# Kernel tuning notes

Measured on AMD Instinct MI355X. Metric: run time of the kernel, lower is better.

## Reference

```python
import jax, jax.numpy as jnp
import numpy as np

B, S, D_IN, UNITS = 8, 2048, 512, 512


def _glorot(key, fan_in, fan_out):
    limit = np.sqrt(6.0 / (fan_in + fan_out)).astype(np.float32)
    return jax.random.uniform(key, (fan_in, fan_out), jnp.float32, -limit, limit)


def setup_inputs() -> dict:
    key = jax.random.key(0)
    kq, kwq, kwv, kwk = jax.random.split(key, 4)
    return {
        "query": jax.random.normal(kq, (B, S, D_IN), jnp.float32),
        "Wq": _glorot(kwq, D_IN, UNITS),   # W_query conv1d k=1, no bias
        "Wv": _glorot(kwv, D_IN, UNITS),   # W_value conv1d k=1, no bias
        "Wk": _glorot(kwk, D_IN, UNITS),   # W_key   conv1d k=1, no bias
    }


def reference(query, Wq, Wv, Wk):
    # Pointwise causal Conv1D(kernel=1, no bias) with sigmoid activation == sigmoid(x @ W)
    q = jax.nn.sigmoid(jnp.einsum('bsd,du->bsu', query, Wq))   # W_query(query)
    k = jax.nn.sigmoid(jnp.einsum('bsd,du->bsu', query, Wv))   # W_value(key=query)
    v = jax.nn.sigmoid(jnp.einsum('bsd,du->bsu', query, Wk))   # W_key(value=query)

    d_in = query.shape[-1]  # scaling uses value's input feature dim, not units
    score = jnp.einsum('bqu,bku->bqk', q, k) / jnp.sqrt(jnp.float32(d_in))  # [B,S,S]

    # Mask: upper triangle INCLUDING diagonal is -inf (strictly-causal, no self)
    s = score.shape[1]
    masked = jnp.where(jnp.triu(jnp.ones((s, s), bool)), -jnp.inf, score)

    # Row 0 is fully masked -> replaced by zeros; rows 1: softmax over j < i
    rest = jax.nn.softmax(masked[:, 1:, :], axis=-1)
    attn = jnp.concatenate([jnp.zeros((score.shape[0], 1, s), score.dtype), rest], axis=1)

    return jnp.einsum('bqk,bku->bqu', attn, v)
```

## Files before the change

kernel.cpp:

```cpp
#include <hip/hip_runtime.h>
#include <stdint.h>


typedef __attribute__((ext_vector_type(4))) float f32x4;
typedef __attribute__((ext_vector_type(8))) short short8;
typedef __attribute__((ext_vector_type(4))) short short4b;

__device__ __forceinline__ short f2bf(float f) {
    union { float f; uint32_t u; } v; v.f = f;
    uint32_t r = (v.u + 0x7FFFu + ((v.u >> 16) & 1u)) >> 16;
    return (short)r;
}
__device__ __forceinline__ float bf2f(short s) {
    union { uint32_t u; float f; } v; v.u = ((uint32_t)(uint16_t)s) << 16; return v.f;
}
__device__ __forceinline__ float sigm(float x) { return 1.0f / (1.0f + __expf(-x)); }

__device__ __forceinline__ void gload_lds16(const void* g, void* l) {
    __builtin_amdgcn_global_load_lds(
        (const __attribute__((address_space(1))) void*)g,
        (__attribute__((address_space(3))) void*)l, 16, 0, 0);
}

#define VMBAR() asm volatile("s_waitcnt vmcnt(0)\n\ts_barrier" ::: "memory")

__global__ __launch_bounds__(256) void convert_x(
    const float* __restrict__ X, short* __restrict__ Xb)
{
    size_t i = (size_t)blockIdx.x * 256 + threadIdx.x;
    const float4* src = reinterpret_cast<const float4*>(X) + i * 2;
    float4 a = src[0], b = src[1];
    short8 o;
    o[0] = f2bf(a.x); o[1] = f2bf(a.y); o[2] = f2bf(a.z); o[3] = f2bf(a.w);
    o[4] = f2bf(b.x); o[5] = f2bf(b.y); o[6] = f2bf(b.z); o[7] = f2bf(b.w);
    *reinterpret_cast<short8*>(Xb + i * 8) = o;
}

__global__ __launch_bounds__(256) void prep_weights(
    const float* __restrict__ Wq, const float* __restrict__ Wv, const float* __restrict__ Wk,
    short* __restrict__ Wt)
{
    __shared__ float T[64 * 68];
    int bid = blockIdx.x;
    int w = bid >> 6;
    int tile = bid & 63;
    int n0 = (tile & 7) * 64;
    int k0 = (tile >> 3) * 64;
    const float* W = (w == 0) ? Wq : (w == 1) ? Wv : Wk;
    int t = threadIdx.x;
    int tr = t >> 4, tc = t & 15;
    for (int rr = 0; rr < 4; ++rr) {
        int row = rr * 16 + tr;
        float4 v = *reinterpret_cast<const float4*>(&W[(size_t)(k0 + row) * 512 + n0 + tc * 4]);
        T[row * 68 + tc * 4 + 0] = v.x;
        T[row * 68 + tc * 4 + 1] = v.y;
        T[row * 68 + tc * 4 + 2] = v.z;
        T[row * 68 + tc * 4 + 3] = v.w;
    }
    __syncthreads();
    for (int wr = 0; wr < 4; ++wr) {
        int nl = wr * 16 + tr;
        short4b o;
        for (int i = 0; i < 4; ++i) o[i] = f2bf(T[(tc * 4 + i) * 68 + nl]);
        *reinterpret_cast<short4b*>(&Wt[((size_t)(w * 512 + n0 + nl)) * 512 + k0 + tc * 4]) = o;
    }
}

__global__ __launch_bounds__(512, 1) void qkv_gemm(
    const short* __restrict__ Xb,
    const short* __restrict__ Wt,
    short* __restrict__ Qb, short* __restrict__ Kb, short* __restrict__ VtG)
{
    __shared__ short SMEM[2][24576];

    int bid = blockIdx.x;
    int xcd = bid & 7;
    int r5 = bid >> 3;
    int mt = xcd * 16 + (r5 & 15);
    int y2 = r5 >> 4;
    int m0 = mt * 128;
    int n2 = y2 * 256;

    int tid = threadIdx.x;
    int wv = tid >> 6, lane = tid & 63;
    int wm = wv >> 2, wn = wv & 3;
    int ln = lane & 15, hi = lane >> 4;

    f32x4 acc[4][4];
#pragma unroll
    for (int i = 0; i < 4; ++i)
#pragma unroll
        for (int j = 0; j < 4; ++j) acc[i][j] = {0.f, 0.f, 0.f, 0.f};

    const short* Asrc = Xb + (size_t)m0 * 512;
    const short* Bsrc = Wt + (size_t)n2 * 512;

#define STAGE(ko, buf)                                                             \
    {                                                                              \
        int _k0 = (ko) * 64;                                                       \
        _Pragma("unroll")                                                          \
        for (int _j = 0; _j < 2; ++_j) {                                           \
            int _r0 = wv * 16 + _j * 8;                                            \
            int _r = _r0 + (lane >> 3);                                            \
            int _sc = ((lane & 7) * 8) ^ ((_r & 7) << 3);                          \
            gload_lds16(Asrc + (size_t)_r * 512 + _k0 + _sc,                       \
                        &SMEM[buf][_r0 * 64]);                                     \
        }                                                                          \
        _Pragma("unroll")                                                          \
        for (int _j = 0; _j < 4; ++_j) {                                           \
            int _r0 = wv * 32 + _j * 8;                                            \
            int _r = _r0 + (lane >> 3);                                            \
            int _sc = ((lane & 7) * 8) ^ ((_r & 7) << 3);                          \
            gload_lds16(Bsrc + (size_t)_r * 512 + _k0 + _sc,                       \
                        &SMEM[buf][8192 + _r0 * 64]);                              \
        }                                                                          \
    }

    STAGE(0, 0);
    for (int ko = 0; ko < 8; ++ko) {
        VMBAR();
        if (ko + 1 < 8) STAGE(ko + 1, (ko + 1) & 1);
        const short* As = SMEM[ko & 1];
        const short* Bs = SMEM[ko & 1] + 8192;
#pragma unroll
        for (int kk = 0; kk < 2; ++kk) {
            int kof = kk * 32 + hi * 8;
            int sw = (ln & 7) << 3;
            short8 af[4], bf[4];
#pragma unroll
            for (int mf = 0; mf < 4; ++mf) {
                int rr = wm * 64 + mf * 16 + ln;
                af[mf] = *reinterpret_cast<const short8*>(&As[rr * 64 + (kof ^ sw)]);
            }
#pragma unroll
            for (int nf = 0; nf < 4; ++nf) {
                int rr = wn * 64 + nf * 16 + ln;
                bf[nf] = *reinterpret_cast<const short8*>(&Bs[rr * 64 + (kof ^ sw)]);
            }
#pragma unroll
            for (int mf = 0; mf < 4; ++mf)
#pragma unroll
                for (int nf = 0; nf < 4; ++nf)
                    acc[mf][nf] = __builtin_amdgcn_mfma_f32_16x16x32_bf16(af[mf], bf[nf], acc[mf][nf], 0, 0, 0);
        }
    }
    __syncthreads();
#undef STAGE

    int w2 = n2 >> 9;
    int nc = n2 & 511;
    short* Ts = SMEM[0];

    if (w2 < 2) {
#pragma unroll
        for (int mf = 0; mf < 4; ++mf)
#pragma unroll
            for (int nf = 0; nf < 4; ++nf)
#pragma unroll
                for (int j = 0; j < 4; ++j) {
                    int rl = wm * 64 + mf * 16 + hi * 4 + j;
                    int cl = wn * 64 + nf * 16 + ln;
                    Ts[rl * 256 + (cl ^ ((rl & 7) << 3))] = f2bf(sigm(acc[mf][nf][j]));
                }
        __syncthreads();
        short* O = (w2 == 0) ? Qb : Kb;
        int rr = tid >> 2, h = tid & 3;
#pragma unroll
        for (int i = 0; i < 8; ++i) {
            int c8 = h * 64 + i * 8;
            short8 v = *reinterpret_cast<const short8*>(&Ts[rr * 256 + (c8 ^ ((rr & 7) << 3))]);
            *reinterpret_cast<short8*>(&O[(size_t)(m0 + rr) * 512 + nc + c8]) = v;
        }
    } else {
#pragma unroll
        for (int mf = 0; mf < 4; ++mf)
#pragma unroll
            for (int nf = 0; nf < 4; ++nf)
#pragma unroll
                for (int j = 0; j < 4; ++j) {
                    int sl = wm * 64 + mf * 16 + hi * 4 + j;
                    int dl = wn * 64 + nf * 16 + ln;
                    Ts[dl * 128 + (sl ^ ((dl & 7) << 3))] = f2bf(sigm(acc[mf][nf][j]));
                }
        __syncthreads();
        int bb = m0 >> 11;
        int s0 = m0 & 2047;
        int d = tid >> 1, h = tid & 1;
#pragma unroll
        for (int i = 0; i < 8; ++i) {
            int s8 = h * 64 + i * 8;
            short8 v = *reinterpret_cast<const short8*>(&Ts[d * 128 + (s8 ^ ((d & 7) << 3))]);
            *reinterpret_cast<short8*>(&VtG[((size_t)(bb * 512 + nc + d)) * 2048 + s0 + s8]) = v;
        }
    }
}

__global__ __launch_bounds__(256, 2) void score_pass(
    const short* __restrict__ Qb, const short* __restrict__ Kb,
    short* __restrict__ Pc, float* __restrict__ Dpart)
{
    __shared__ short SMEM[2][16384];
    __shared__ float psum[2][128];

    const float scale = 0.044194173824159216f;

    int bid = blockIdx.x;
    int b = bid & 7;
    int idx = bid >> 3;
    int ti = 0;
    while ((ti + 1) * (ti + 2) / 2 <= idx) ++ti;
    int tj = idx - ti * (ti + 1) / 2;
    int m0 = ti * 128, n0 = tj * 128;

    int tid = threadIdx.x;
    int w = tid >> 6, lane = tid & 63;
    int wr = w >> 1, wc = w & 1;
    int ln = lane & 15, hi = lane >> 4;

    const short* Qsrc = Qb + (size_t)b * 2048 * 512 + (size_t)m0 * 512;
    const short* Ksrc = Kb + (size_t)b * 2048 * 512 + (size_t)n0 * 512;

    f32x4 acc[4][4];
#pragma unroll
    for (int i = 0; i < 4; ++i)
#pragma unroll
        for (int j = 0; j < 4; ++j) acc[i][j] = {0.f, 0.f, 0.f, 0.f};

    int srow = w * 8 + (lane >> 3);
    int ssc0 = (lane & 7) * 8;

#define SSTAGE(ko, buf)                                                            \
    {                                                                              \
        int _k0 = (ko) * 64;                                                       \
        _Pragma("unroll")                                                          \
        for (int _j = 0; _j < 4; ++_j) {                                           \
            int _r = srow + _j * 32;                                               \
            int _sc = ssc0 ^ ((_r & 7) << 3);                                      \
            gload_lds16(Qsrc + (size_t)_r * 512 + _k0 + _sc,                       \
                        &SMEM[buf][(w * 8 + _j * 32) * 64]);                       \
        }                                                                          \
        _Pragma("unroll")                                                          \
        for (int _j = 0; _j < 4; ++_j) {                                           \
            int _r = srow + _j * 32;                                               \
            int _sc = ssc0 ^ ((_r & 7) << 3);                                      \
            gload_lds16(Ksrc + (size_t)_r * 512 + _k0 + _sc,                       \
                        &SMEM[buf][8192 + (w * 8 + _j * 32) * 64]);                \
        }                                                                          \
    }

    SSTAGE(0, 0);
    for (int ko = 0; ko < 8; ++ko) {
        VMBAR();
        if (ko + 1 < 8) SSTAGE(ko + 1, (ko + 1) & 1);
        const short* As = SMEM[ko & 1];
        const short* Bs = SMEM[ko & 1] + 8192;
#pragma unroll
        for (int kk = 0; kk < 2; ++kk) {
            int kof = kk * 32 + hi * 8;
            int sw = (ln & 7) << 3;
            short8 af[4], bf[4];
#pragma unroll
            for (int mf = 0; mf < 4; ++mf)
                af[mf] = *reinterpret_cast<const short8*>(&As[(wr * 64 + mf * 16 + ln) * 64 + (kof ^ sw)]);
#pragma unroll
            for (int nf = 0; nf < 4; ++nf)
                bf[nf] = *reinterpret_cast<const short8*>(&Bs[(wc * 64 + nf * 16 + ln) * 64 + (kof ^ sw)]);
#pragma unroll
            for (int mf = 0; mf < 4; ++mf)
#pragma unroll
                for (int nf = 0; nf < 4; ++nf)
                    acc[mf][nf] = __builtin_amdgcn_mfma_f32_16x16x32_bf16(af[mf], bf[nf], acc[mf][nf], 0, 0, 0);
        }
    }
    __syncthreads();
#undef SSTAGE

    short* Ts = SMEM[0];
#pragma unroll
    for (int mf = 0; mf < 4; ++mf) {
        float rs[4] = {0.f, 0.f, 0.f, 0.f};
#pragma unroll
        for (int nf = 0; nf < 4; ++nf)
#pragma unroll
            for (int j = 0; j < 4; ++j) {
                int rl = wr * 64 + mf * 16 + hi * 4 + j;
                int cl = wc * 64 + nf * 16 + ln;
                int irow = m0 + rl, jcol = n0 + cl;
                float p = (jcol < irow) ? __expf(acc[mf][nf][j] * scale) : 0.f;
                short hs = f2bf(p);
                Ts[rl * 128 + (cl ^ ((rl & 7) << 3))] = hs;
                rs[j] += bf2f(hs);
            }
#pragma unroll
        for (int j = 0; j < 4; ++j) {
            float s = rs[j];
            s += __shfl_xor(s, 1);
            s += __shfl_xor(s, 2);
            s += __shfl_xor(s, 4);
            s += __shfl_xor(s, 8);
            if (ln == 0) psum[wc][wr * 64 + mf * 16 + hi * 4 + j] = s;
        }
    }
    __syncthreads();
    short* Ptile = Pc + (size_t)(b * 136 + idx) * 128 * 128;
    {
        int r = tid >> 1, h = tid & 1;
#pragma unroll
        for (int i = 0; i < 8; ++i) {
            int c8 = h * 64 + i * 8;
            short8 v = *reinterpret_cast<const short8*>(&Ts[r * 128 + (c8 ^ ((r & 7) << 3))]);
            *reinterpret_cast<short8*>(&Ptile[(size_t)r * 128 + c8]) = v;
        }
    }
    if (tid < 128)
        Dpart[((size_t)b * 16 + tj) * 2048 + m0 + tid] = psum[0][tid] + psum[1][tid];
}

__global__ __launch_bounds__(256) void pv_pass(
    const short* __restrict__ Pc, const short* __restrict__ VtG,
    const float* __restrict__ Dpart, float* __restrict__ Out)
{
    __shared__ short SMEM[2][12288];
    __shared__ float dnm[128];

    int bid = blockIdx.x;
    int b = bid & 7;
    int rr = bid >> 3;
    int grp = rr >> 5, off = rr & 31;
    int ti = (grp & 1) ? (15 - (off >> 1)) : (off >> 1);
    int colhalf = 2 * grp + (off & 1);
    int m0 = ti * 128, n0 = colhalf * 64;

    int tid = threadIdx.x;
    int w = tid >> 6, lane = tid & 63;
    int wr = w >> 1, wc = w & 1;
    int ln = lane & 15, hi = lane >> 4;

    if (tid < 128) {
        float s = 0.f;
        for (int tj = 0; tj <= ti; ++tj)
            s += Dpart[((size_t)b * 16 + tj) * 2048 + m0 + tid];
        int gi = m0 + tid;
        dnm[tid] = (gi == 0) ? 0.f : 1.0f / s;
    }

    const short* Ptiles = Pc + (size_t)(b * 136 + ti * (ti + 1) / 2) * 128 * 128;
    const short* Vsrc = VtG + (size_t)b * 512 * 2048 + (size_t)n0 * 2048;

    f32x4 acc[4][2];
#pragma unroll
    for (int i = 0; i < 4; ++i)
#pragma unroll
        for (int j = 0; j < 2; ++j) acc[i][j] = {0.f, 0.f, 0.f, 0.f};

    int srow = w * 8 + (lane >> 3);
    int ssc0 = (lane & 7) * 8;
    int nks = 2 * (ti + 1);

#define PSTAGE(ks, buf)                                                            \
    {                                                                              \
        int _tj = (ks) >> 1;                                                       \
        int _j0 = ((ks) & 1) * 64;                                                 \
        const short* _Pt = Ptiles + (size_t)_tj * 128 * 128;                       \
        _Pragma("unroll")                                                          \
        for (int _j = 0; _j < 4; ++_j) {                                           \
            int _r = srow + _j * 32;                                               \
            int _sc = ssc0 ^ ((_r & 7) << 3);                                      \
            gload_lds16(_Pt + (size_t)_r * 128 + _j0 + _sc,                        \
                        &SMEM[buf][(w * 8 + _j * 32) * 64]);                       \
        }                                                                          \
        _Pragma("unroll")                                                          \
        for (int _j = 0; _j < 2; ++_j) {                                           \
            int _r = srow + _j * 32;                                               \
            int _sc = ssc0 ^ ((_r & 7) << 3);                                      \
            gload_lds16(Vsrc + (size_t)_r * 2048 + _tj * 128 + _j0 + _sc,          \
                        &SMEM[buf][8192 + (w * 8 + _j * 32) * 64]);                \
        }                                                                          \
    }

    PSTAGE(0, 0);
    for (int ks = 0; ks < nks; ++ks) {
        VMBAR();
        if (ks + 1 < nks) PSTAGE(ks + 1, (ks + 1) & 1);
        const short* As = SMEM[ks & 1];
        const short* Bs = SMEM[ks & 1] + 8192;
#pragma unroll
        for (int kk = 0; kk < 2; ++kk) {
            int kof = kk * 32 + hi * 8;
            int sw = (ln & 7) << 3;
            short8 af[4], bf[2];
#pragma unroll
            for (int mf = 0; mf < 4; ++mf)
                af[mf] = *reinterpret_cast<const short8*>(&As[(wr * 64 + mf * 16 + ln) * 64 + (kof ^ sw)]);
#pragma unroll
            for (int nf = 0; nf < 2; ++nf)
                bf[nf] = *reinterpret_cast<const short8*>(&Bs[(wc * 32 + nf * 16 + ln) * 64 + (kof ^ sw)]);
#pragma unroll
            for (int mf = 0; mf < 4; ++mf)
#pragma unroll
                for (int nf = 0; nf < 2; ++nf)
                    acc[mf][nf] = __builtin_amdgcn_mfma_f32_16x16x32_bf16(af[mf], bf[nf], acc[mf][nf], 0, 0, 0);
        }
    }
    __syncthreads();
#undef PSTAGE

    float* Tf = reinterpret_cast<float*>(SMEM);
#pragma unroll
    for (int mf = 0; mf < 4; ++mf)
#pragma unroll
        for (int nf = 0; nf < 2; ++nf)
#pragma unroll
            for (int j = 0; j < 4; ++j) {
                int rl = wr * 64 + mf * 16 + hi * 4 + j;
                int cl = wc * 32 + nf * 16 + ln;
                Tf[rl * 64 + (cl ^ ((rl & 7) << 2))] = acc[mf][nf][j] * dnm[rl];
            }
    __syncthreads();
    {
        int r = tid >> 1, h = tid & 1;
        float* orow = Out + ((size_t)b * 2048 + m0 + r) * 512 + n0;
#pragma unroll
        for (int i = 0; i < 8; ++i) {
            int c4 = (h * 8 + i) * 4;
            float4 v = *reinterpret_cast<const float4*>(&Tf[r * 64 + (c4 ^ ((r & 7) << 2))]);
            *reinterpret_cast<float4*>(&orow[c4]) = v;
        }
    }
}

extern "C" void kernel_launch(void* const* d_in, const int* in_sizes, int n_in,
                              void* d_out, int out_size, void* d_ws, size_t ws_size,
                              hipStream_t stream) {
    const float* X  = (const float*)d_in[0];
    const float* Wq = (const float*)d_in[1];
    const float* Wv = (const float*)d_in[2];
    const float* Wk = (const float*)d_in[3];
    float* Out = (float*)d_out;

    char* ws = (char*)d_ws;
    const size_t WT_BYTES  = (size_t)3 * 512 * 512 * 2;
    const size_t MAT_BYTES = (size_t)16384 * 512 * 2;
    const size_t PC_BYTES  = (size_t)8 * 136 * 128 * 128 * 2;
    short* Wt = (short*)ws;
    short* Qb = (short*)(ws + WT_BYTES);
    short* Kb = (short*)(ws + WT_BYTES + MAT_BYTES);
    short* Vt = (short*)(ws + WT_BYTES + 2 * MAT_BYTES);
    short* Pc = (short*)(ws + WT_BYTES + 3 * MAT_BYTES);
    short* Xb = Pc;
    float* Dp = (float*)(ws + WT_BYTES + 3 * MAT_BYTES + PC_BYTES);

    convert_x<<<4096, 256, 0, stream>>>(X, Xb);
    prep_weights<<<192, 256, 0, stream>>>(Wq, Wv, Wk, Wt);
    qkv_gemm<<<768, 512, 0, stream>>>(Xb, Wt, Qb, Kb, Vt);
    score_pass<<<1088, 256, 0, stream>>>(Qb, Kb, Pc, Dp);
    pv_pass<<<1024, 256, 0, stream>>>(Pc, Vt, Dp, Out);
}
```

Measured before the change: 153.2 us.

## Triple-buffer QKV GEMM with split B-half staging and priority-boosted MFMA phases

```diff
diff --git a/kernel.cpp b/kernel.cpp
--- a/kernel.cpp
+++ b/kernel.cpp
@@ -71,85 +71,115 @@
     const short* __restrict__ Wt,
     short* __restrict__ Qb, short* __restrict__ Kb, short* __restrict__ VtG)
 {
-    __shared__ short SMEM[2][24576];
+    __shared__ short SMEM[3][24576];
 
     int bid = blockIdx.x;
-    int xcd = bid & 7;
-    int r5 = bid >> 3;
-    int mt = xcd * 16 + (r5 & 15);
-    int y2 = r5 >> 4;
+    int nt2 = bid >> 7;
+    int mt = bid & 127;
     int m0 = mt * 128;
-    int n2 = y2 * 256;
+    int n2 = nt2 * 256;
 
     int tid = threadIdx.x;
     int wv = tid >> 6, lane = tid & 63;
     int wm = wv >> 2, wn = wv & 3;
     int ln = lane & 15, hi = lane >> 4;
 
-    f32x4 acc[4][4];
-#pragma unroll
-    for (int i = 0; i < 4; ++i)
-#pragma unroll
-        for (int j = 0; j < 4; ++j) acc[i][j] = {0.f, 0.f, 0.f, 0.f};
-
     const short* Asrc = Xb + (size_t)m0 * 512;
     const short* Bsrc = Wt + (size_t)n2 * 512;
 
-#define STAGE(ko, buf)                                                             \
-    {                                                                              \
-        int _k0 = (ko) * 64;                                                       \
-        _Pragma("unroll")                                                          \
-        for (int _j = 0; _j < 2; ++_j) {                                           \
-            int _r0 = wv * 16 + _j * 8;                                            \
-            int _r = _r0 + (lane >> 3);                                            \
-            int _sc = ((lane & 7) * 8) ^ ((_r & 7) << 3);                          \
-            gload_lds16(Asrc + (size_t)_r * 512 + _k0 + _sc,                       \
-                        &SMEM[buf][_r0 * 64]);                                     \
-        }                                                                          \
-        _Pragma("unroll")                                                          \
-        for (int _j = 0; _j < 4; ++_j) {                                           \
-            int _r0 = wv * 32 + _j * 8;                                            \
-            int _r = _r0 + (lane >> 3);                                            \
-            int _sc = ((lane & 7) * 8) ^ ((_r & 7) << 3);                          \
-            gload_lds16(Bsrc + (size_t)_r * 512 + _k0 + _sc,                       \
-                        &SMEM[buf][8192 + _r0 * 64]);                              \
-        }                                                                          \
-    }
-
-    STAGE(0, 0);
-    for (int ko = 0; ko < 8; ++ko) {
-        VMBAR();
-        if (ko + 1 < 8) STAGE(ko + 1, (ko + 1) & 1);
-        const short* As = SMEM[ko & 1];
-        const short* Bs = SMEM[ko & 1] + 8192;
-#pragma unroll
-        for (int kk = 0; kk < 2; ++kk) {
-            int kof = kk * 32 + hi * 8;
-            int sw = (ln & 7) << 3;
-            short8 af[4], bf[4];
+    auto stageA = [&](int kt, int buf) {
+#pragma unroll
+        for (int j = 0; j < 2; ++j) {
+            int r0 = wv * 16 + j * 8;
+            int r = r0 + (lane >> 3);
+            gload_lds16(Asrc + (size_t)r * 512 + kt * 64 + (((lane & 7) * 8) ^ ((r & 7) << 3)),
+                        &SMEM[buf][r0 * 64]);
+        }
+    };
+    auto stageBH = [&](int kt, int h, int buf) {
+#pragma unroll
+        for (int j = 0; j < 2; ++j) {
+            int r0 = h * 128 + wv * 16 + j * 8;
+            int r = r0 + (lane >> 3);
+            gload_lds16(Bsrc + (size_t)r * 512 + kt * 64 + (((lane & 7) * 8) ^ ((r & 7) << 3)),
+                        &SMEM[buf][8192 + r0 * 64]);
+        }
+    };
+
+    f32x4 acc[4][4];
+#pragma unroll
+    for (int i = 0; i < 4; ++i)
+#pragma unroll
+        for (int j = 0; j < 4; ++j) acc[i][j] = {0.f, 0.f, 0.f, 0.f};
+
+    stageA(0, 0); stageBH(0, 0, 0); stageBH(0, 1, 0);
+    stageA(1, 1); stageBH(1, 0, 1); stageBH(1, 1, 1);
+    asm volatile("s_waitcnt vmcnt(6)\n\ts_barrier" ::: "memory");
+
+    int sw = (ln & 7) << 3;
+    for (int t = 0; t < 8; ++t) {
+        int bufc = t % 3;
+        const short* As = SMEM[bufc];
+        const short* Bsb = SMEM[bufc] + 8192;
+        int b2 = (t + 2) % 3;
+        bool st = (t + 2) < 8;
+
+        short8 af[2][4];
+#pragma unroll
+        for (int kk = 0; kk < 2; ++kk)
 #pragma unroll
             for (int mf = 0; mf < 4; ++mf) {
-                int rr = wm * 64 + mf * 16 + ln;
-                af[mf] = *reinterpret_cast<const short8*>(&As[rr * 64 + (kof ^ sw)]);
+                int r = wm * 64 + mf * 16 + ln;
+                af[kk][mf] = *reinterpret_cast<const short8*>(&As[r * 64 + ((kk * 32 + hi * 8) ^ sw)]);
             }
-#pragma unroll
-            for (int nf = 0; nf < 4; ++nf) {
-                int rr = wn * 64 + nf * 16 + ln;
-                bf[nf] = *reinterpret_cast<const short8*>(&Bs[rr * 64 + (kof ^ sw)]);
+
+        short8 bfr[2][2];
+#pragma unroll
+        for (int kk = 0; kk < 2; ++kk)
+#pragma unroll
+            for (int nf = 0; nf < 2; ++nf) {
+                int r = wn * 64 + nf * 16 + ln;
+                bfr[kk][nf] = *reinterpret_cast<const short8*>(&Bsb[r * 64 + ((kk * 32 + hi * 8) ^ sw)]);
             }
-#pragma unroll
-            for (int mf = 0; mf < 4; ++mf)
-#pragma unroll
-                for (int nf = 0; nf < 4; ++nf)
-                    acc[mf][nf] = __builtin_amdgcn_mfma_f32_16x16x32_bf16(af[mf], bf[nf], acc[mf][nf], 0, 0, 0);
-        }
-    }
-    __syncthreads();
-#undef STAGE
-
-    int w2 = n2 >> 9;
-    int nc = n2 & 511;
-    short* Ts = SMEM[0];
+        if (st) { stageA(t + 2, b2); stageBH(t + 2, 0, b2); }
+        asm volatile("s_barrier" ::: "memory");
+        __builtin_amdgcn_s_setprio(1);
+#pragma unroll
+        for (int kk = 0; kk < 2; ++kk)
+#pragma unroll
+            for (int mf = 0; mf < 4; ++mf)
+#pragma unroll
+                for (int nf = 0; nf < 2; ++nf)
+                    acc[mf][nf] = __builtin_amdgcn_mfma_f32_16x16x32_bf16(af[kk][mf], bfr[kk][nf], acc[mf][nf], 0, 0, 0);
+        __builtin_amdgcn_s_setprio(0);
+        asm volatile("s_barrier" ::: "memory");
+
+#pragma unroll
+        for (int kk = 0; kk < 2; ++kk)
+#pragma unroll
+            for (int nf = 0; nf < 2; ++nf) {
+                int r = wn * 64 + (2 + nf) * 16 + ln;
+                bfr[kk][nf] = *reinterpret_cast<const short8*>(&Bsb[r * 64 + ((kk * 32 + hi * 8) ^ sw)]);
+            }
+        if (st) stageBH(t + 2, 1, b2);
+        if (t <= 5) asm volatile("s_waitcnt vmcnt(6)\n\ts_barrier" ::: "memory");
+        else        asm volatile("s_waitcnt vmcnt(0)\n\ts_barrier" ::: "memory");
+        __builtin_amdgcn_s_setprio(1);
+#pragma unroll
+        for (int kk = 0; kk < 2; ++kk)
+#pragma unroll
+            for (int mf = 0; mf < 4; ++mf)
+#pragma unroll
+                for (int nf = 0; nf < 2; ++nf)
+                    acc[mf][2 + nf] = __builtin_amdgcn_mfma_f32_16x16x32_bf16(af[kk][mf], bfr[kk][nf], acc[mf][2 + nf], 0, 0, 0);
+        __builtin_amdgcn_s_setprio(0);
+        asm volatile("s_barrier" ::: "memory");
+    }
+    __syncthreads();
+
+    int w2 = nt2 >> 1;
+    int nc = (nt2 & 1) * 256;
+    short* Ts = &SMEM[0][0];
 
     if (w2 < 2) {
 #pragma unroll
```

Result: no change. 152.1 us (-0.7%).

## Enlarge QKV and score GEMM tiles to 256x256 with 512-thread blocks

Applied to the files above, without the earlier changes.

```diff
diff --git a/kernel.cpp b/kernel.cpp
--- a/kernel.cpp
+++ b/kernel.cpp
@@ -71,36 +71,28 @@
     const short* __restrict__ Wt,
     short* __restrict__ Qb, short* __restrict__ Kb, short* __restrict__ VtG)
 {
-    __shared__ short SMEM[2][24576];
+    __shared__ short SMEM[2][32768];
 
     int bid = blockIdx.x;
-    int xcd = bid & 7;
-    int r5 = bid >> 3;
-    int mt = xcd * 16 + (r5 & 15);
-    int y2 = r5 >> 4;
-    int m0 = mt * 128;
-    int n2 = y2 * 256;
+    int nt2 = bid >> 6;
+    int mt = bid & 63;
+    int m0 = mt * 256;
+    int n2 = nt2 * 256;
 
     int tid = threadIdx.x;
     int wv = tid >> 6, lane = tid & 63;
     int wm = wv >> 2, wn = wv & 3;
     int ln = lane & 15, hi = lane >> 4;
 
-    f32x4 acc[4][4];
-#pragma unroll
-    for (int i = 0; i < 4; ++i)
-#pragma unroll
-        for (int j = 0; j < 4; ++j) acc[i][j] = {0.f, 0.f, 0.f, 0.f};
-
     const short* Asrc = Xb + (size_t)m0 * 512;
     const short* Bsrc = Wt + (size_t)n2 * 512;
 
-#define STAGE(ko, buf)                                                             \
+#define QSTG(ko, buf)                                                              \
     {                                                                              \
         int _k0 = (ko) * 64;                                                       \
         _Pragma("unroll")                                                          \
-        for (int _j = 0; _j < 2; ++_j) {                                           \
-            int _r0 = wv * 16 + _j * 8;                                            \
+        for (int _j = 0; _j < 4; ++_j) {                                           \
+            int _r0 = wv * 32 + _j * 8;                                            \
             int _r = _r0 + (lane >> 3);                                            \
             int _sc = ((lane & 7) * 8) ^ ((_r & 7) << 3);                          \
             gload_lds16(Asrc + (size_t)_r * 512 + _k0 + _sc,                       \
@@ -112,183 +104,189 @@
             int _r = _r0 + (lane >> 3);                                            \
             int _sc = ((lane & 7) * 8) ^ ((_r & 7) << 3);                          \
             gload_lds16(Bsrc + (size_t)_r * 512 + _k0 + _sc,                       \
-                        &SMEM[buf][8192 + _r0 * 64]);                              \
-        }                                                                          \
-    }
-
-    STAGE(0, 0);
+                        &SMEM[buf][16384 + _r0 * 64]);                             \
+        }                                                                          \
+    }
+
+    f32x4 acc[8][4];
+#pragma unroll
+    for (int i = 0; i < 8; ++i)
+#pragma unroll
+        for (int j = 0; j < 4; ++j) acc[i][j] = {0.f, 0.f, 0.f, 0.f};
+
+    QSTG(0, 0);
+    int sw = (ln & 7) << 3;
     for (int ko = 0; ko < 8; ++ko) {
         VMBAR();
-        if (ko + 1 < 8) STAGE(ko + 1, (ko + 1) & 1);
+        if (ko + 1 < 8) QSTG(ko + 1, (ko + 1) & 1);
         const short* As = SMEM[ko & 1];
-        const short* Bs = SMEM[ko & 1] + 8192;
+        const short* Bs = SMEM[ko & 1] + 16384;
 #pragma unroll
         for (int kk = 0; kk < 2; ++kk) {
-            int kof = kk * 32 + hi * 8;
-            int sw = (ln & 7) << 3;
-            short8 af[4], bf[4];
-#pragma unroll
-            for (int mf = 0; mf < 4; ++mf) {
-                int rr = wm * 64 + mf * 16 + ln;
-                af[mf] = *reinterpret_cast<const short8*>(&As[rr * 64 + (kof ^ sw)]);
-            }
+            int kof = (kk * 32 + hi * 8) ^ sw;
+            short8 bf[4];
 #pragma unroll
             for (int nf = 0; nf < 4; ++nf) {
-                int rr = wn * 64 + nf * 16 + ln;
-                bf[nf] = *reinterpret_cast<const short8*>(&Bs[rr * 64 + (kof ^ sw)]);
-            }
-#pragma unroll
-            for (int mf = 0; mf < 4; ++mf)
+                int r = wn * 64 + nf * 16 + ln;
+                bf[nf] = *reinterpret_cast<const short8*>(&Bs[r * 64 + kof]);
+            }
+#pragma unroll
+            for (int mf = 0; mf < 8; ++mf) {
+                int r = wm * 128 + mf * 16 + ln;
+                short8 af = *reinterpret_cast<const short8*>(&As[r * 64 + kof]);
 #pragma unroll
                 for (int nf = 0; nf < 4; ++nf)
-                    acc[mf][nf] = __builtin_amdgcn_mfma_f32_16x16x32_bf16(af[mf], bf[nf], acc[mf][nf], 0, 0, 0);
-        }
-    }
-    __syncthreads();
-#undef STAGE
-
-    int w2 = n2 >> 9;
-    int nc = n2 & 511;
-    short* Ts = SMEM[0];
+                    acc[mf][nf] = __builtin_amdgcn_mfma_f32_16x16x32_bf16(af, bf[nf], acc[mf][nf], 0, 0, 0);
+            }
+        }
+    }
+    __syncthreads();
+#undef QSTG
+
+    int w2 = nt2 >> 1;
+    int nc = (nt2 & 1) * 256;
+    short* Ts = &SMEM[0][0];
 
     if (w2 < 2) {
 #pragma unroll
-        for (int mf = 0; mf < 4; ++mf)
+        for (int mf = 0; mf < 8; ++mf)
 #pragma unroll
             for (int nf = 0; nf < 4; ++nf)
 #pragma unroll
                 for (int j = 0; j < 4; ++j) {
-                    int rl = wm * 64 + mf * 16 + hi * 4 + j;
+                    int rl = wm * 128 + mf * 16 + hi * 4 + j;
                     int cl = wn * 64 + nf * 16 + ln;
                     Ts[rl * 256 + (cl ^ ((rl & 7) << 3))] = f2bf(sigm(acc[mf][nf][j]));
                 }
         __syncthreads();
         short* O = (w2 == 0) ? Qb : Kb;
-        int rr = tid >> 2, h = tid & 3;
-#pragma unroll
-        for (int i = 0; i < 8; ++i) {
-            int c8 = h * 64 + i * 8;
-            short8 v = *reinterpret_cast<const short8*>(&Ts[rr * 256 + (c8 ^ ((rr & 7) << 3))]);
-            *reinterpret_cast<short8*>(&O[(size_t)(m0 + rr) * 512 + nc + c8]) = v;
+        int r = tid >> 1, h = tid & 1;
+#pragma unroll
+        for (int i = 0; i < 16; ++i) {
+            int c8 = h * 128 + i * 8;
+            short8 v = *reinterpret_cast<const short8*>(&Ts[r * 256 + (c8 ^ ((r & 7) << 3))]);
+            *reinterpret_cast<short8*>(&O[(size_t)(m0 + r) * 512 + nc + c8]) = v;
         }
     } else {
 #pragma unroll
-        for (int mf = 0; mf < 4; ++mf)
+        for (int mf = 0; mf < 8; ++mf)
 #pragma unroll
             for (int nf = 0; nf < 4; ++nf)
 #pragma unroll
                 for (int j = 0; j < 4; ++j) {
-                    int sl = wm * 64 + mf * 16 + hi * 4 + j;
+                    int sl = wm * 128 + mf * 16 + hi * 4 + j;
                     int dl = wn * 64 + nf * 16 + ln;
-                    Ts[dl * 128 + (sl ^ ((dl & 7) << 3))] = f2bf(sigm(acc[mf][nf][j]));
+                    Ts[dl * 256 + (sl ^ ((dl & 7) << 3))] = f2bf(sigm(acc[mf][nf][j]));
                 }
         __syncthreads();
         int bb = m0 >> 11;
         int s0 = m0 & 2047;
         int d = tid >> 1, h = tid & 1;
 #pragma unroll
-        for (int i = 0; i < 8; ++i) {
-            int s8 = h * 64 + i * 8;
-            short8 v = *reinterpret_cast<const short8*>(&Ts[d * 128 + (s8 ^ ((d & 7) << 3))]);
+        for (int i = 0; i < 16; ++i) {
+            int s8 = h * 128 + i * 8;
+            short8 v = *reinterpret_cast<const short8*>(&Ts[d * 256 + (s8 ^ ((d & 7) << 3))]);
             *reinterpret_cast<short8*>(&VtG[((size_t)(bb * 512 + nc + d)) * 2048 + s0 + s8]) = v;
         }
     }
 }
 
-__global__ __launch_bounds__(256, 2) void score_pass(
+__global__ __launch_bounds__(512, 1) void score_pass(
     const short* __restrict__ Qb, const short* __restrict__ Kb,
     short* __restrict__ Pc, float* __restrict__ Dpart)
 {
-    __shared__ short SMEM[2][16384];
-    __shared__ float psum[2][128];
+    __shared__ short SMEM[2][32768];
+    __shared__ float psum[2][2][256];
 
     const float scale = 0.044194173824159216f;
 
     int bid = blockIdx.x;
     int b = bid & 7;
     int idx = bid >> 3;
-    int ti = 0;
-    while ((ti + 1) * (ti + 2) / 2 <= idx) ++ti;
-    int tj = idx - ti * (ti + 1) / 2;
-    int m0 = ti * 128, n0 = tj * 128;
+    int ti2 = 0;
+    while ((ti2 + 1) * (ti2 + 2) / 2 <= idx) ++ti2;
+    int tj2 = idx - ti2 * (ti2 + 1) / 2;
+    int m0 = ti2 * 256, n0 = tj2 * 256;
 
     int tid = threadIdx.x;
-    int w = tid >> 6, lane = tid & 63;
-    int wr = w >> 1, wc = w & 1;
+    int wv = tid >> 6, lane = tid & 63;
+    int wm = wv >> 2, wn = wv & 3;
     int ln = lane & 15, hi = lane >> 4;
 
-    const short* Qsrc = Qb + (size_t)b * 2048 * 512 + (size_t)m0 * 512;
-    const short* Ksrc = Kb + (size_t)b * 2048 * 512 + (size_t)n0 * 512;
-
-    f32x4 acc[4][4];
-#pragma unroll
-    for (int i = 0; i < 4; ++i)
-#pragma unroll
-        for (int j = 0; j < 4; ++j) acc[i][j] = {0.f, 0.f, 0.f, 0.f};
-
-    int srow = w * 8 + (lane >> 3);
-    int ssc0 = (lane & 7) * 8;
-
-#define SSTAGE(ko, buf)                                                            \
+    const short* Asrc = Qb + (size_t)b * 2048 * 512 + (size_t)m0 * 512;
+    const short* Bsrc = Kb + (size_t)b * 2048 * 512 + (size_t)n0 * 512;
+
+#define SSTG(ko, buf)                                                              \
     {                                                                              \
         int _k0 = (ko) * 64;                                                       \
         _Pragma("unroll")                                                          \
         for (int _j = 0; _j < 4; ++_j) {                                           \
-            int _r = srow + _j * 32;                                               \
-            int _sc = ssc0 ^ ((_r & 7) << 3);                                      \
-            gload_lds16(Qsrc + (size_t)_r * 512 + _k0 + _sc,                       \
-                        &SMEM[buf][(w * 8 + _j * 32) * 64]);                       \
+            int _r0 = wv * 32 + _j * 8;                                            \
+            int _r = _r0 + (lane >> 3);                                            \
+            int _sc = ((lane & 7) * 8) ^ ((_r & 7) << 3);                          \
+            gload_lds16(Asrc + (size_t)_r * 512 + _k0 + _sc,                       \
+                        &SMEM[buf][_r0 * 64]);                                     \
         }                                                                          \
         _Pragma("unroll")                                                          \
         for (int _j = 0; _j < 4; ++_j) {                                           \
-            int _r = srow + _j * 32;                                               \
-            int _sc = ssc0 ^ ((_r & 7) << 3);                                      \
-            gload_lds16(Ksrc + (size_t)_r * 512 + _k0 + _sc,                       \
-                        &SMEM[buf][8192 + (w * 8 + _j * 32) * 64]);                \
-        }                                                                          \
-    }
-
-    SSTAGE(0, 0);
+            int _r0 = wv * 32 + _j * 8;                                            \
+            int _r = _r0 + (lane >> 3);                                            \
+            int _sc = ((lane & 7) * 8) ^ ((_r & 7) << 3);                          \
+            gload_lds16(Bsrc + (size_t)_r * 512 + _k0 + _sc,                       \
+                        &SMEM[buf][16384 + _r0 * 64]);                             \
+        }                                                                          \
+    }
+
+    f32x4 acc[8][4];
+#pragma unroll
+    for (int i = 0; i < 8; ++i)
+#pragma unroll
+        for (int j = 0; j < 4; ++j) acc[i][j] = {0.f, 0.f, 0.f, 0.f};
+
+    SSTG(0, 0);
+    int sw = (ln & 7) << 3;
     for (int ko = 0; ko < 8; ++ko) {
         VMBAR();
-        if (ko + 1 < 8) SSTAGE(ko + 1, (ko + 1) & 1);
+        if (ko + 1 < 8) SSTG(ko + 1, (ko + 1) & 1);
         const short* As = SMEM[ko & 1];
-        const short* Bs = SMEM[ko & 1] + 8192;
+        const short* Bs = SMEM[ko & 1] + 16384;
 #pragma unroll
         for (int kk = 0; kk < 2; ++kk) {
-            int kof = kk * 32 + hi * 8;
-            int sw = (ln & 7) << 3;
-            short8 af[4], bf[4];
-#pragma unroll
-            for (int mf = 0; mf < 4; ++mf)
-                af[mf] = *reinterpret_cast<const short8*>(&As[(wr * 64 + mf * 16 + ln) * 64 + (kof ^ sw)]);
-#pragma unroll
-            for (int nf = 0; nf < 4; ++nf)
-                bf[nf] = *reinterpret_cast<const short8*>(&Bs[(wc * 64 + nf * 16 + ln) * 64 + (kof ^ sw)]);
-#pragma unroll
-            for (int mf = 0; mf < 4; ++mf)
+            int kof = (kk * 32 + hi * 8) ^ sw;
+            short8 bf[4];
+#pragma unroll
+            for (int nf = 0; nf < 4; ++nf) {
+                int r = wn * 64 + nf * 16 + ln;
+                bf[nf] = *reinterpret_cast<const short8*>(&Bs[r * 64 + kof]);
+            }
+#pragma unroll
+            for (int mf = 0; mf < 8; ++mf) {
+                int r = wm * 128 + mf * 16 + ln;
+                short8 af = *reinterpret_cast<const short8*>(&As[r * 64 + kof]);
 #pragma unroll
                 for (int nf = 0; nf < 4; ++nf)
-                    acc[mf][nf] = __builtin_amdgcn_mfma_f32_16x16x32_bf16(af[mf], bf[nf], acc[mf][nf], 0, 0, 0);
-        }
-    }
-    __syncthreads();
-#undef SSTAGE
-
-    short* Ts = SMEM[0];
-#pragma unroll
-    for (int mf = 0; mf < 4; ++mf) {
+                    acc[mf][nf] = __builtin_amdgcn_mfma_f32_16x16x32_bf16(af, bf[nf], acc[mf][nf], 0, 0, 0);
+            }
+        }
+    }
+    __syncthreads();
+#undef SSTG
+
+    short* Ts = &SMEM[0][0];
+    int h = wn >> 1;
+#pragma unroll
+    for (int mf = 0; mf < 8; ++mf) {
         float rs[4] = {0.f, 0.f, 0.f, 0.f};
 #pragma unroll
         for (int nf = 0; nf < 4; ++nf)
 #pragma unroll
             for (int j = 0; j < 4; ++j) {
-                int rl = wr * 64 + mf * 16 + hi * 4 + j;
-                int cl = wc * 64 + nf * 16 + ln;
+                int rl = wm * 128 + mf * 16 + hi * 4 + j;
+                int cl = wn * 64 + nf * 16 + ln;
                 int irow = m0 + rl, jcol = n0 + cl;
                 float p = (jcol < irow) ? __expf(acc[mf][nf][j] * scale) : 0.f;
                 short hs = f2bf(p);
-                Ts[rl * 128 + (cl ^ ((rl & 7) << 3))] = hs;
+                Ts[rl * 256 + (cl ^ ((rl & 7) << 3))] = hs;
                 rs[j] += bf2f(hs);
             }
 #pragma unroll
@@ -298,22 +296,38 @@
             s += __shfl_xor(s, 2);
             s += __shfl_xor(s, 4);
             s += __shfl_xor(s, 8);
-            if (ln == 0) psum[wc][wr * 64 + mf * 16 + hi * 4 + j] = s;
-        }
-    }
-    __syncthreads();
-    short* Ptile = Pc + (size_t)(b * 136 + idx) * 128 * 128;
+            if (ln == 0) psum[h][wn & 1][wm * 128 + mf * 16 + hi * 4 + j] = s;
+        }
+    }
+    __syncthreads();
+
     {
-        int r = tid >> 1, h = tid & 1;
-#pragma unroll
-        for (int i = 0; i < 8; ++i) {
-            int c8 = h * 64 + i * 8;
-            short8 v = *reinterpret_cast<const short8*>(&Ts[r * 128 + (c8 ^ ((r & 7) << 3))]);
-            *reinterpret_cast<short8*>(&Ptile[(size_t)r * 128 + c8]) = v;
-        }
-    }
-    if (tid < 128)
-        Dpart[((size_t)b * 16 + tj) * 2048 + m0 + tid] = psum[0][tid] + psum[1][tid];
+        int h2 = tid >> 8, row = tid & 255;
+        Dpart[((size_t)b * 16 + 2 * tj2 + h2) * 2048 + m0 + row] =
+            psum[h2][0][row] + psum[h2][1][row];
+    }
+
+    {
+        int r = tid >> 2, q = tid & 3;
+#pragma unroll
+        for (int a = 0; a < 2; ++a)
+#pragma unroll
+            for (int c = 0; c < 2; ++c) {
+                int ti128 = 2 * ti2 + a;
+                int tj128 = 2 * tj2 + c;
+                if (tj128 > ti128) continue;
+                short* Ptile = Pc + (size_t)(b * 136 + ti128 * (ti128 + 1) / 2 + tj128) * 16384;
+                int rl = a * 128 + r;
+#pragma unroll
+                for (int i = 0; i < 4; ++i) {
+                    int c8 = q * 32 + i * 8;
+                    int cl = c * 128 + c8;
+                    short8 v = *reinterpret_cast<const short8*>(
+                        &Ts[rl * 256 + (cl ^ ((rl & 7) << 3))]);
+                    *reinterpret_cast<short8*>(&Ptile[(size_t)r * 128 + c8]) = v;
+                }
+            }
+    }
 }
 
 __global__ __launch_bounds__(256) void pv_pass(
@@ -452,7 +466,7 @@
 
     convert_x<<<4096, 256, 0, stream>>>(X, Xb);
     prep_weights<<<192, 256, 0, stream>>>(Wq, Wv, Wk, Wt);
-    qkv_gemm<<<768, 512, 0, stream>>>(Xb, Wt, Qb, Kb, Vt);
-    score_pass<<<1088, 256, 0, stream>>>(Qb, Kb, Pc, Dp);
+    qkv_gemm<<<384, 512, 0, stream>>>(Xb, Wt, Qb, Kb, Vt);
+    score_pass<<<288, 512, 0, stream>>>(Qb, Kb, Pc, Dp);
     pv_pass<<<1024, 256, 0, stream>>>(Pc, Vt, Dp, Out);
 }
```

After: 181.5 us. 18.5% more time.
